# Performance work log

Hardware: AMD Instinct MI355X
Metric: run time of the kernel (lower is better)

The kernel has to match this reference:

```python
import jax, jax.numpy as jnp
import numpy as np

T, B, C = 1024, 16, 1024
H, K, PAD = 16, 7, 6  # num_heads, kernel_size, padding_l (causal)
R = C // H


def setup_inputs() -> dict:
    key = jax.random.key(0)
    kx, kw = jax.random.split(key)
    x = jax.random.normal(kx, (T, B, C), dtype=jnp.float32)
    # xavier_uniform for weight_linear.weight of shape (H*K, C)
    bound = float(np.sqrt(6.0 / (C + H * K)))
    W = jax.random.uniform(kw, (H * K, C), dtype=jnp.float32, minval=-bound, maxval=bound)
    return {"x": x, "W": W}


def reference(x, W):
    Tn, Bn, Cn = x.shape
    # dynamic per-position conv weights: (T, B, H, K)
    w = jnp.einsum('tbc,oc->tbo', x, W).reshape(Tn, Bn, H, K)

    # band structure: row t attends absolute positions t + k - PAD, k in [0, K)
    pos = jnp.arange(Tn)[:, None] + jnp.arange(K)[None, :] - PAD     # (T, K)
    valid = (pos >= 0) & (pos < Tn)                                   # (T, K)
    logits = jnp.where(valid[:, None, None, :], w, -jnp.inf)
    wsm = jax.nn.softmax(logits, axis=-1)                             # (T, B, H, K), zeros off-band

    # windowed weighted sum (the bmm against the band matrix, done directly)
    pc = jnp.clip(pos, 0, Tn - 1)                                     # (T, K)
    xh = x.reshape(Tn, Bn, H, R)
    xg = xh[pc]                                                       # (T, K, B, H, R)
    out = jnp.einsum('tbhk,tkbhr->tbhr', wsm, xg).reshape(Tn, Bn, Cn)

    # dense (B*H, T, T) softmaxed band matrix, as returned by the torch module
    w_bht = wsm.transpose(1, 2, 0, 3).reshape(Bn * H, Tn, K)
    dense = jnp.zeros((Bn * H, Tn, Tn), wsm.dtype)
    dense = dense.at[:, jnp.arange(Tn)[:, None], pc].add(jnp.where(valid, w_bht, 0.0))
    return out, dense
```

## Files before the change

### kernel.cpp

```cpp
#include <hip/hip_runtime.h>
#include <math.h>

#define TT 1024
#define BB 16
#define CC 1024
#define HH 16
#define KK 7
#define PADL 6
#define HK 112
#define LSTRIDE 116

typedef short bf16x8 __attribute__((ext_vector_type(8)));
typedef float f32x4 __attribute__((ext_vector_type(4)));

__device__ __forceinline__ short f2bf(float f) {
    union { float f; unsigned u; } v; v.f = f;
    unsigned r = v.u + 0x7fff + ((v.u >> 16) & 1);
    return (short)(r >> 16);
}

__global__ __launch_bounds__(256) void k0_cvtW(const float* __restrict__ W,
                                               short* __restrict__ Wb) {
    const int i = (blockIdx.x * 256 + threadIdx.x) * 8;
    const float4 a0 = *(const float4*)(W + i);
    const float4 a1 = *(const float4*)(W + i + 4);
    bf16x8 v;
    v[0] = f2bf(a0.x); v[1] = f2bf(a0.y); v[2] = f2bf(a0.z); v[3] = f2bf(a0.w);
    v[4] = f2bf(a1.x); v[5] = f2bf(a1.y); v[6] = f2bf(a1.z); v[7] = f2bf(a1.w);
    *(bf16x8*)(Wb + i) = v;
}

__global__ __launch_bounds__(256) void k1_mfma(const float* __restrict__ x,
                                               const short* __restrict__ Wb,
                                               float* __restrict__ wsm) {
    __shared__ __align__(16) float Llog[4][16 * LSTRIDE];
    __shared__ __align__(16) float Lout[4][16 * HK];

    const int tid = threadIdx.x;
    const int w = tid >> 6;
    const int lane = tid & 63;
    const int quad = lane >> 4;
    const int lr = lane & 15;
    const int strip = blockIdx.x * 4 + w;
    const int r0 = strip * 16;

    bf16x8 ap, bp;
#pragma unroll
    for (int e = 0; e < 8; ++e) {
        const int k = quad * 8 + e;
        ap[e] = (k == lr) ? (short)0x3F80 : (short)0;
        bp[e] = f2bf((float)k);
    }
    f32x4 pz = (f32x4){0.f, 0.f, 0.f, 0.f};
    pz = __builtin_amdgcn_mfma_f32_16x16x32_bf16(ap, bp, pz, 0, 0, 0);
    const bool claim = (pz[0] == (float)(quad * 4)) &&
                       (pz[1] == (float)(quad * 4 + 1));

    const float* __restrict__ xa = x + (size_t)(r0 + lr) * CC + quad * 8;
    const short* __restrict__ wb = Wb + (size_t)lr * CC + quad * 8;

    f32x4 acc[7];
#pragma unroll
    for (int j = 0; j < 7; ++j) acc[j] = (f32x4){0.f, 0.f, 0.f, 0.f};

#pragma unroll 4
    for (int k0 = 0; k0 < CC; k0 += 32) {
        const float4 a0 = *(const float4*)(xa + k0);
        const float4 a1 = *(const float4*)(xa + k0 + 4);
        bf16x8 af;
        af[0] = f2bf(a0.x); af[1] = f2bf(a0.y); af[2] = f2bf(a0.z); af[3] = f2bf(a0.w);
        af[4] = f2bf(a1.x); af[5] = f2bf(a1.y); af[6] = f2bf(a1.z); af[7] = f2bf(a1.w);
#pragma unroll
        for (int j = 0; j < 7; ++j) {
            const bf16x8 bfrag = *(const bf16x8*)(wb + (size_t)(j * 16) * CC + k0);
            acc[j] = __builtin_amdgcn_mfma_f32_16x16x32_bf16(af, bfrag, acc[j], 0, 0, 0);
        }
    }

#pragma unroll
    for (int j = 0; j < 7; ++j)
#pragma unroll
        for (int r = 0; r < 4; ++r) {
            const int rowi = claim ? (quad * 4 + r) : lr;
            const int coli = claim ? lr : (quad * 4 + r);
            Llog[w][rowi * LSTRIDE + j * 16 + coli] = acc[j][r];
        }
    __syncthreads();

    const int kmin = (strip >= PADL) ? 0 : (PADL - strip);
#pragma unroll
    for (int p = 0; p < 4; ++p) {
        const int idx = p * 64 + lane;
        const int m = idx >> 4;
        const int h = idx & 15;
        const float* lp = &Llog[w][m * LSTRIDE + h * KK];
        float a[KK];
#pragma unroll
        for (int k = 0; k < KK; ++k) a[k] = lp[k];

        float mx = -INFINITY;
#pragma unroll
        for (int k = 0; k < KK; ++k)
            if (k >= kmin) mx = fmaxf(mx, a[k]);
        float e[KK], s = 0.f;
#pragma unroll
        for (int k = 0; k < KK; ++k) {
            if (k >= kmin) { e[k] = expf(a[k] - mx); s += e[k]; }
            else           { e[k] = 0.f; }
        }
        const float inv = 1.f / s;
        float* op = &Lout[w][m * HK + h * KK];
#pragma unroll
        for (int k = 0; k < KK; ++k) op[k] = e[k] * inv;
    }
    __syncthreads();

    float* __restrict__ dst = wsm + (size_t)r0 * HK;
    const float* __restrict__ src = &Lout[w][0];
#pragma unroll
    for (int i = 0; i < 7; ++i) {
        const int o = i * 256 + lane * 4;
        *(float4*)(dst + o) = *(const float4*)(src + o);
    }
}

__global__ __launch_bounds__(256) void k23_fused(const float* __restrict__ x,
                                                 const float* __restrict__ wsm,
                                                 float* __restrict__ dense,
                                                 float* __restrict__ out) {
    const int blk = blockIdx.x;

    if ((blk % 5) == 0) {
        const int r0 = (blk / 5) << 2;
        const int t = r0 >> 4;
        const int c = threadIdx.x << 2;
        const int h = c >> 6;
        const int kmin = (t >= PADL) ? 0 : (PADL - t);

#pragma unroll
        for (int i = 0; i < 4; ++i) {
            const int row = r0 + i;
            const float* __restrict__ wp = wsm + ((size_t)row * HH + h) * KK;
            float w[KK];
#pragma unroll
            for (int k = 0; k < KK; ++k) w[k] = wp[k];

            f32x4 acc = (f32x4){0.f, 0.f, 0.f, 0.f};
            for (int k = kmin; k < KK; ++k) {
                const f32x4 xv = *(const f32x4*)(
                    x + ((size_t)row + (size_t)(k - PADL) * BB) * CC + c);
                acc[0] += w[k] * xv[0];
                acc[1] += w[k] * xv[1];
                acc[2] += w[k] * xv[2];
                acc[3] += w[k] * xv[3];
            }
            *(f32x4*)(out + (size_t)row * CC + c) = acc;
        }
    } else {
        const int blk2 = blk - (blk / 5) - 1;
        const int bh = blk2 >> 6;
        const int tc = blk2 & 63;
        const int b = bh >> 4;
        const int h = bh & 15;
        const int t0 = tc * 16;
        const int tid = threadIdx.x;

        const int r = tid & 15;
        const int j = tid >> 4;
        const int t = t0 + r;
        const int cc = t - PADL + j;
        float bandv = 0.f;
        bool bandon = (j < KK) && (cc >= 0);
        if (bandon)
            bandv = wsm[(((size_t)t * BB + b) * HH + h) * KK + j];

        float* __restrict__ drow =
            dense + ((size_t)bh * TT + t0) * TT + (tid << 2);
        const f32x4 z = (f32x4){0.f, 0.f, 0.f, 0.f};
#pragma unroll
        for (int i = 0; i < 16; ++i) {
            *(f32x4*)drow = z;
            drow += TT;
        }

        __syncthreads();
        if (bandon)
            dense[((size_t)bh * TT + t) * TT + cc] = bandv;
    }
}

extern "C" void kernel_launch(void* const* d_in, const int* in_sizes, int n_in,
                              void* d_out, int out_size, void* d_ws, size_t ws_size,
                              hipStream_t stream) {
    const float* x = (const float*)d_in[0];
    const float* W = (const float*)d_in[1];
    float* out = (float*)d_out;
    float* dense = out + (size_t)TT * BB * CC;
    float* wsm = (float*)d_ws;
    short* Wb = (short*)(wsm + (size_t)TT * BB * HK);

    k0_cvtW<<<56, 256, 0, stream>>>(W, Wb);
    k1_mfma<<<256, 256, 0, stream>>>(x, Wb, wsm);
    k23_fused<<<5 * (TT * BB) / 4, 256, 0, stream>>>(x, wsm, dense, out);
}
```

Measured before the change: 1.228 ms.

## Split fused kernel into memset, band scatter and output kernels

Zeroing of the 1 GiB dense band matrix moves from a custom kernel to hipMemsetAsync. The band values are then written by a separate scatter kernel, and the windowed weighted sum becomes its own kernel that uses nontemporal stores. The aim is to hit peak write bandwidth via the driver fill path and drop the in-kernel barrier. In exchange it adds launches and a scattered write pass that touches the dense rows again after the memset.

After: 1.206 ms. About the same (-1.8%).

```diff
diff --git a/kernel.cpp b/kernel.cpp
--- a/kernel.cpp
+++ b/kernel.cpp
@@ -124,68 +124,52 @@
     }
 }
 
-__global__ __launch_bounds__(256) void k23_fused(const float* __restrict__ x,
-                                                 const float* __restrict__ wsm,
-                                                 float* __restrict__ dense,
-                                                 float* __restrict__ out) {
-    const int blk = blockIdx.x;
+__global__ __launch_bounds__(256) void k2_scatter(const float* __restrict__ wsm,
+                                                  float* __restrict__ dense) {
+    const int idx = blockIdx.x * 256 + threadIdx.x;
+    const float v = wsm[idx];
 
-    if ((blk % 5) == 0) {
-        const int r0 = (blk / 5) << 2;
-        const int t = r0 >> 4;
-        const int c = threadIdx.x << 2;
-        const int h = c >> 6;
-        const int kmin = (t >= PADL) ? 0 : (PADL - t);
+    const int j = idx % KK;
+    const int rem = idx / KK;
+    const int h = rem & 15;
+    const int rem2 = rem >> 4;
+    const int b = rem2 & 15;
+    const int t = rem2 >> 4;
+
+    const int cc = t + j - PADL;
+    if (cc >= 0) {
+        const int bh = b * HH + h;
+        dense[((size_t)bh * TT + t) * TT + cc] = v;
+    }
+}
+
+__global__ __launch_bounds__(256) void k3_out(const float* __restrict__ x,
+                                              const float* __restrict__ wsm,
+                                              float* __restrict__ out) {
+    const int r0 = blockIdx.x << 2;
+    const int t = r0 >> 4;
+    const int c = threadIdx.x << 2;
+    const int h = c >> 6;
+    const int kmin = (t >= PADL) ? 0 : (PADL - t);
 
 #pragma unroll
-        for (int i = 0; i < 4; ++i) {
-            const int row = r0 + i;
-            const float* __restrict__ wp = wsm + ((size_t)row * HH + h) * KK;
-            float w[KK];
+    for (int i = 0; i < 4; ++i) {
+        const int row = r0 + i;
+        const float* __restrict__ wp = wsm + ((size_t)row * HH + h) * KK;
+        float w[KK];
 #pragma unroll
-            for (int k = 0; k < KK; ++k) w[k] = wp[k];
+        for (int k = 0; k < KK; ++k) w[k] = wp[k];
 
-            f32x4 acc = (f32x4){0.f, 0.f, 0.f, 0.f};
-            for (int k = kmin; k < KK; ++k) {
-                const f32x4 xv = *(const f32x4*)(
-                    x + ((size_t)row + (size_t)(k - PADL) * BB) * CC + c);
-                acc[0] += w[k] * xv[0];
-                acc[1] += w[k] * xv[1];
-                acc[2] += w[k] * xv[2];
-                acc[3] += w[k] * xv[3];
-            }
-            *(f32x4*)(out + (size_t)row * CC + c) = acc;
+        f32x4 acc = (f32x4){0.f, 0.f, 0.f, 0.f};
+        for (int k = kmin; k < KK; ++k) {
+            const f32x4 xv = *(const f32x4*)(
+                x + ((size_t)row + (size_t)(k - PADL) * BB) * CC + c);
+            acc[0] += w[k] * xv[0];
+            acc[1] += w[k] * xv[1];
+            acc[2] += w[k] * xv[2];
+            acc[3] += w[k] * xv[3];
         }
-    } else {
-        const int blk2 = blk - (blk / 5) - 1;
-        const int bh = blk2 >> 6;
-        const int tc = blk2 & 63;
-        const int b = bh >> 4;
-        const int h = bh & 15;
-        const int t0 = tc * 16;
-        const int tid = threadIdx.x;
-
-        const int r = tid & 15;
-        const int j = tid >> 4;
-        const int t = t0 + r;
-        const int cc = t - PADL + j;
-        float bandv = 0.f;
-        bool bandon = (j < KK) && (cc >= 0);
-        if (bandon)
-            bandv = wsm[(((size_t)t * BB + b) * HH + h) * KK + j];
-
-        float* __restrict__ drow =
-            dense + ((size_t)bh * TT + t0) * TT + (tid << 2);
-        const f32x4 z = (f32x4){0.f, 0.f, 0.f, 0.f};
-#pragma unroll
-        for (int i = 0; i < 16; ++i) {
-            *(f32x4*)drow = z;
-            drow += TT;
-        }
-
-        __syncthreads();
-        if (bandon)
-            dense[((size_t)bh * TT + t) * TT + cc] = bandv;
+        __builtin_nontemporal_store(acc, (f32x4*)(out + (size_t)row * CC + c));
     }
 }
 
@@ -199,7 +183,10 @@
     float* wsm = (float*)d_ws;
     short* Wb = (short*)(wsm + (size_t)TT * BB * HK);
 
+    hipMemsetAsync(dense, 0, (size_t)BB * HH * TT * TT * sizeof(float), stream);
+
     k0_cvtW<<<56, 256, 0, stream>>>(W, Wb);
     k1_mfma<<<256, 256, 0, stream>>>(x, Wb, wsm);
-    k23_fused<<<5 * (TT * BB) / 4, 256, 0, stream>>>(x, wsm, dense, out);
+    k2_scatter<<<(TT * BB * HK) / 256, 256, 0, stream>>>(wsm, dense);
+    k3_out<<<(TT * BB) / 4, 256, 0, stream>>>(x, wsm, out);
 }
```
